# Kernel optimization log

Hardware: AMD Instinct MI355X
Metric: run time of the kernel (lower is better)

## Reference

```python
import jax, jax.numpy as jnp
import numpy as np

K = 0.1  # curvature (called k in the module)
EPS = 1e-15

def setup_inputs() -> dict:
    key = jax.random.key(0)
    k1, k2, k3 = jax.random.split(key, 3)
    B, C, D = 2048, 1000, 64
    x = jax.random.normal(k1, (B, D), dtype=jnp.float32) * 0.05  # inside ball
    a_vals = jax.random.normal(k2, (C, D), dtype=jnp.float32) * 0.05
    p_vals = jax.random.normal(k3, (C, D), dtype=jnp.float32) * 0.05
    return {"x": x, "a_vals": a_vals, "p_vals": p_vals}

def reference(x, a_vals, p_vals):
    k = jnp.asarray(K, dtype=x.dtype)
    sqrt_k = jnp.sqrt(k)
    # poincare_exp0: exponential map at the origin
    p_norm = jnp.maximum(jnp.linalg.norm(p_vals, axis=1, keepdims=True), EPS)  # [C,1]
    p_poin = jnp.tanh(sqrt_k * p_norm) * p_vals / (sqrt_k * p_norm)            # [C,D]
    # conformal scaling of a (as written in the module: 1 + k*||p||^2)
    p2 = jnp.sum(p_poin * p_poin, axis=1)                                      # [C]
    a_poin = a_vals * (1.0 + k * p2)[:, None]                                  # [C,D]
    # hyperbolic softmax logits
    lam = 2.0 / (1.0 - k * p2)                                                 # [C]
    a_norm = jnp.maximum(jnp.linalg.norm(a_poin, axis=1), EPS)                 # [C]
    scale = lam * a_norm / sqrt_k                                              # [C]
    # mobius addition of (-p) (+) x, batched -> [C,B,D]
    mp = -p_poin                                                               # [C,D]
    xy = jnp.einsum('cd,bd->cb', mp, x)                                        # [C,B]
    x2 = jnp.sum(mp * mp, axis=-1)[:, None]                                    # [C,1]
    y2 = jnp.sum(x * x, axis=-1)[None, :]                                      # [1,B]
    num = ((1.0 + 2.0 * k * xy + k * y2)[..., None] * mp[:, None, :]
           + (1.0 - k * x2)[..., None] * x[None, :, :])                        # [C,B,D]
    den = 1.0 + 2.0 * k * xy + (k * k) * x2 * y2                               # [C,B]
    mob = num / den[..., None]                                                 # [C,B,D]
    numer = 2.0 * sqrt_k * jnp.einsum('cbd,cd->cb', mob, a_poin)               # [C,B]
    denom = a_norm[:, None] * (1.0 - k * jnp.sum(mob * mob, axis=-1))          # [C,B]
    logits = scale[:, None] * jnp.arcsinh(numer / denom)                       # [C,B]
    return logits.T                                                            # [B,C]
```

## Files before the change

kernel.cpp:

```cpp
#include <hip/hip_runtime.h>
#include <hip/hip_bf16.h>
#include <math.h>

#define KCURV  0.1f
#define KK     0.010000001f
#define SQRT_K 0.31622776601683794f
#define TWO_SQRT_K 0.6324555320336759f
#define INV_SQRT_K 3.1622776601683795f
#define TD 64

typedef __bf16  bf16x8  __attribute__((ext_vector_type(8)));
typedef float   f32x4   __attribute__((ext_vector_type(4)));

__device__ __forceinline__ unsigned short f2bf(float f) {
    __hip_bfloat16 h = __float2bfloat16(f);
    return *(unsigned short*)&h;
}

__global__ __launch_bounds__(256) void prep_kernel(
    const float* __restrict__ a_vals, const float* __restrict__ p_vals,
    unsigned short* __restrict__ Pbf, unsigned short* __restrict__ Abf,
    float* __restrict__ x2g, float* __restrict__ pag,
    float* __restrict__ ang, float* __restrict__ scg,
    int C)
{
    const int tid  = threadIdx.x;
    const int item = blockIdx.x * 64 + (tid >> 2);
    const int q    = tid & 3;
    const int gc   = item < C ? item : C - 1;

    const float* pr = p_vals + (size_t)gc * TD + q * 16;
    const float* ar = a_vals + (size_t)gc * TD + q * 16;
    float pv[16], av[16];
    #pragma unroll
    for (int m = 0; m < 4; ++m) {
        *(float4*)&pv[m * 4] = *(const float4*)(pr + m * 4);
        *(float4*)&av[m * 4] = *(const float4*)(ar + m * 4);
    }
    float s_pp = 0.f, s_aa = 0.f, s_pa = 0.f;
    #pragma unroll
    for (int u = 0; u < 16; ++u) {
        s_pp = fmaf(pv[u], pv[u], s_pp);
        s_aa = fmaf(av[u], av[u], s_aa);
        s_pa = fmaf(pv[u], av[u], s_pa);
    }
    s_pp += __shfl_xor(s_pp, 1, 64); s_pp += __shfl_xor(s_pp, 2, 64);
    s_aa += __shfl_xor(s_aa, 1, 64); s_aa += __shfl_xor(s_aa, 2, 64);
    s_pa += __shfl_xor(s_pa, 1, 64); s_pa += __shfl_xor(s_pa, 2, 64);

    float pn = sqrtf(s_pp); if (pn < 1e-15f) pn = 1e-15f;
    float arg = SQRT_K * pn;
    float t = tanhf(arg);
    float factor = t / arg;
    float p2 = factor * factor * s_pp;
    float ca = 1.0f + KCURV * p2;
    float anorm = ca * sqrtf(s_aa); if (anorm < 1e-15f) anorm = 1e-15f;
    float lam = 2.0f / (1.0f - KCURV * p2);
    float scale = lam * anorm * INV_SQRT_K;
    float pa = -factor * ca * s_pa;

    if (q == 0) {
        x2g[item] = p2; pag[item] = pa; ang[item] = anorm; scg[item] = scale;
    }
    unsigned short ubp[16], uba[16];
    #pragma unroll
    for (int u = 0; u < 16; ++u) {
        ubp[u] = f2bf(-factor * pv[u]);
        uba[u] = f2bf(ca * av[u]);
    }
    unsigned short* dp = Pbf + (size_t)item * TD + q * 16;
    unsigned short* da = Abf + (size_t)item * TD + q * 16;
    *(ulonglong2*)dp       = *(const ulonglong2*)&ubp[0];
    *(ulonglong2*)(dp + 8) = *(const ulonglong2*)&ubp[8];
    *(ulonglong2*)da       = *(const ulonglong2*)&uba[0];
    *(ulonglong2*)(da + 8) = *(const ulonglong2*)&uba[8];
}

__global__ __launch_bounds__(256) void mlr_gemm_kernel(
    const float* __restrict__ x,
    const unsigned short* __restrict__ Pbf, const unsigned short* __restrict__ Abf,
    const float* __restrict__ x2g, const float* __restrict__ pag,
    const float* __restrict__ ang, const float* __restrict__ scg,
    float* __restrict__ out, int B, int C)
{
    const int tid  = threadIdx.x;
    const int w    = tid >> 6;
    const int lane = tid & 63;
    const int m16  = lane & 15;
    const int quad = lane >> 4;
    const int cb   = blockIdx.x * 64;
    const int rb   = blockIdx.y * 64;
    int arow = rb + 16 * w + m16; if (arow >= B) arow = B - 1;

    float xv[2][8];
    bf16x8 bp[4][2], ba[4][2];
    #pragma unroll
    for (int step = 0; step < 2; ++step) {
        const int ko = quad * 8 + step * 32;
        const float* xr = x + (size_t)arow * TD + ko;
        *(float4*)&xv[step][0] = *(const float4*)xr;
        *(float4*)&xv[step][4] = *(const float4*)(xr + 4);
        #pragma unroll
        for (int t = 0; t < 4; ++t) {
            const size_t crow = (size_t)(cb + 16 * t + m16) * TD + ko;
            bp[t][step] = *(const bf16x8*)(Pbf + crow);
            ba[t][step] = *(const bf16x8*)(Abf + crow);
        }
    }

    float s = 0.f;
    #pragma unroll
    for (int step = 0; step < 2; ++step)
        #pragma unroll
        for (int u = 0; u < 8; ++u) s = fmaf(xv[step][u], xv[step][u], s);
    s += __shfl_xor(s, 16, 64);
    s += __shfl_xor(s, 32, 64);
    float y2r[4];
    #pragma unroll
    for (int r = 0; r < 4; ++r) y2r[r] = __shfl(s, quad * 4 + r, 64);

    bf16x8 af[2];
    #pragma unroll
    for (int step = 0; step < 2; ++step) {
        union { unsigned short u[8]; bf16x8 v; } cv;
        #pragma unroll
        for (int u = 0; u < 8; ++u) cv.u[u] = f2bf(xv[step][u]);
        af[step] = cv.v;
    }

    f32x4 accP[4], accA[4];
    #pragma unroll
    for (int t = 0; t < 4; ++t) {
        accP[t] = (f32x4){0.f, 0.f, 0.f, 0.f};
        accA[t] = (f32x4){0.f, 0.f, 0.f, 0.f};
    }
    #pragma unroll
    for (int step = 0; step < 2; ++step) {
        #pragma unroll
        for (int t = 0; t < 4; ++t) {
            accP[t] = __builtin_amdgcn_mfma_f32_16x16x32_bf16(af[step], bp[t][step], accP[t], 0, 0, 0);
            accA[t] = __builtin_amdgcn_mfma_f32_16x16x32_bf16(af[step], ba[t][step], accA[t], 0, 0, 0);
        }
    }

    #pragma unroll
    for (int t = 0; t < 4; ++t) {
        const int cl = cb + 16 * t + m16;
        const float x2 = x2g[cl], pa = pag[cl], an = ang[cl], sc = scg[cl];
        const float beta = 1.0f - KCURV * x2;
        const float kkx2 = KK * x2;
        #pragma unroll
        for (int r = 0; r < 4; ++r) {
            const int gr = rb + 16 * w + quad * 4 + r;
            const float y2 = y2r[r];
            const float xy = accP[t][r];
            const float xa = accA[t][r];
            float t1    = fmaf(2.0f * KCURV, xy, 1.0f);
            float den   = fmaf(kkx2, y2, t1);
            float alpha = fmaf(KCURV, y2, t1);
            float g     = fmaf(alpha, pa, beta * xa);
            float M     = fmaf(alpha * alpha, x2,
                          fmaf(2.0f * alpha * beta, xy, beta * beta * y2));
            float dd    = fmaf(den, den, -KCURV * M);
            float z     = TWO_SQRT_K * g * den * __builtin_amdgcn_rcpf(an * dd);
            float lg    = sc * __logf(z + sqrtf(fmaf(z, z, 1.0f)));
            if (cl < C && gr < B) out[(size_t)gr * C + cl] = lg;
        }
    }
}

extern "C" void kernel_launch(void* const* d_in, const int* in_sizes, int n_in,
                              void* d_out, int out_size, void* d_ws, size_t ws_size,
                              hipStream_t stream) {
    const float* x      = (const float*)d_in[0];
    const float* a_vals = (const float*)d_in[1];
    const float* p_vals = (const float*)d_in[2];
    const int B = in_sizes[0] / TD;
    const int C = in_sizes[1] / TD;
    const int rowBlocks = (B + 63) / 64;
    const int clsBlocks = (C + 63) / 64;
    const int CPAD = clsBlocks * 64;

    char* ws = (char*)d_ws;
    unsigned short* Pbf = (unsigned short*)ws;
    unsigned short* Abf = (unsigned short*)(ws + (size_t)CPAD * TD * 2);
    float* x2g = (float*)(ws + (size_t)CPAD * TD * 4);
    float* pag = x2g + CPAD;
    float* ang = pag + CPAD;
    float* scg = ang + CPAD;

    prep_kernel<<<clsBlocks, 256, 0, stream>>>(
        a_vals, p_vals, Pbf, Abf, x2g, pag, ang, scg, C);

    dim3 grid(clsBlocks, rowBlocks);
    mlr_gemm_kernel<<<grid, dim3(256), 0, stream>>>(
        x, Pbf, Abf, x2g, pag, ang, scg, (float*)d_out, B, C);
}
```

Measured before the change: 70.17 us.

## Fuse class-parameter prep into GEMM kernel, removing separate prep launch

Removes the separate prep kernel and its workspace round-trip. Each GEMM block now loads the fp32 p/a rows itself, computes the norms, tanh factor and scalars, and converts to bf16 in registers. tanhf is replaced by an exp/rcp formula with a small-argument series. This drops one launch and the global writes and reads of the intermediates. In exchange every one of the 32 row-blocks recomputes the same class prep, and each wave repeats it, adding redundant fp32 loads and ALU work.

```diff
diff --git a/kernel.cpp b/kernel.cpp
--- a/kernel.cpp
+++ b/kernel.cpp
@@ -17,70 +17,10 @@
     return *(unsigned short*)&h;
 }
 
-__global__ __launch_bounds__(256) void prep_kernel(
-    const float* __restrict__ a_vals, const float* __restrict__ p_vals,
-    unsigned short* __restrict__ Pbf, unsigned short* __restrict__ Abf,
-    float* __restrict__ x2g, float* __restrict__ pag,
-    float* __restrict__ ang, float* __restrict__ scg,
-    int C)
-{
-    const int tid  = threadIdx.x;
-    const int item = blockIdx.x * 64 + (tid >> 2);
-    const int q    = tid & 3;
-    const int gc   = item < C ? item : C - 1;
-
-    const float* pr = p_vals + (size_t)gc * TD + q * 16;
-    const float* ar = a_vals + (size_t)gc * TD + q * 16;
-    float pv[16], av[16];
-    #pragma unroll
-    for (int m = 0; m < 4; ++m) {
-        *(float4*)&pv[m * 4] = *(const float4*)(pr + m * 4);
-        *(float4*)&av[m * 4] = *(const float4*)(ar + m * 4);
-    }
-    float s_pp = 0.f, s_aa = 0.f, s_pa = 0.f;
-    #pragma unroll
-    for (int u = 0; u < 16; ++u) {
-        s_pp = fmaf(pv[u], pv[u], s_pp);
-        s_aa = fmaf(av[u], av[u], s_aa);
-        s_pa = fmaf(pv[u], av[u], s_pa);
-    }
-    s_pp += __shfl_xor(s_pp, 1, 64); s_pp += __shfl_xor(s_pp, 2, 64);
-    s_aa += __shfl_xor(s_aa, 1, 64); s_aa += __shfl_xor(s_aa, 2, 64);
-    s_pa += __shfl_xor(s_pa, 1, 64); s_pa += __shfl_xor(s_pa, 2, 64);
-
-    float pn = sqrtf(s_pp); if (pn < 1e-15f) pn = 1e-15f;
-    float arg = SQRT_K * pn;
-    float t = tanhf(arg);
-    float factor = t / arg;
-    float p2 = factor * factor * s_pp;
-    float ca = 1.0f + KCURV * p2;
-    float anorm = ca * sqrtf(s_aa); if (anorm < 1e-15f) anorm = 1e-15f;
-    float lam = 2.0f / (1.0f - KCURV * p2);
-    float scale = lam * anorm * INV_SQRT_K;
-    float pa = -factor * ca * s_pa;
-
-    if (q == 0) {
-        x2g[item] = p2; pag[item] = pa; ang[item] = anorm; scg[item] = scale;
-    }
-    unsigned short ubp[16], uba[16];
-    #pragma unroll
-    for (int u = 0; u < 16; ++u) {
-        ubp[u] = f2bf(-factor * pv[u]);
-        uba[u] = f2bf(ca * av[u]);
-    }
-    unsigned short* dp = Pbf + (size_t)item * TD + q * 16;
-    unsigned short* da = Abf + (size_t)item * TD + q * 16;
-    *(ulonglong2*)dp       = *(const ulonglong2*)&ubp[0];
-    *(ulonglong2*)(dp + 8) = *(const ulonglong2*)&ubp[8];
-    *(ulonglong2*)da       = *(const ulonglong2*)&uba[0];
-    *(ulonglong2*)(da + 8) = *(const ulonglong2*)&uba[8];
-}
-
-__global__ __launch_bounds__(256) void mlr_gemm_kernel(
+__global__ __launch_bounds__(256) void fused_mlr_kernel(
     const float* __restrict__ x,
-    const unsigned short* __restrict__ Pbf, const unsigned short* __restrict__ Abf,
-    const float* __restrict__ x2g, const float* __restrict__ pag,
-    const float* __restrict__ ang, const float* __restrict__ scg,
+    const float* __restrict__ a_vals,
+    const float* __restrict__ p_vals,
     float* __restrict__ out, int B, int C)
 {
     const int tid  = threadIdx.x;
@@ -93,19 +33,67 @@
     int arow = rb + 16 * w + m16; if (arow >= B) arow = B - 1;
 
     float xv[2][8];
-    bf16x8 bp[4][2], ba[4][2];
     #pragma unroll
     for (int step = 0; step < 2; ++step) {
         const int ko = quad * 8 + step * 32;
         const float* xr = x + (size_t)arow * TD + ko;
         *(float4*)&xv[step][0] = *(const float4*)xr;
         *(float4*)&xv[step][4] = *(const float4*)(xr + 4);
+    }
+
+    bf16x8 bp[4][2], ba[4][2];
+    float x2s[4], pas[4], ans[4], scs[4];
+    #pragma unroll
+    for (int t = 0; t < 4; ++t) {
+        int c = cb + 16 * t + m16; if (c >= C) c = C - 1;
+        const float* pr = p_vals + (size_t)c * TD + quad * 8;
+        const float* ar = a_vals + (size_t)c * TD + quad * 8;
+        float pv[16], av[16];
+        *(float4*)&pv[0]  = *(const float4*)pr;
+        *(float4*)&pv[4]  = *(const float4*)(pr + 4);
+        *(float4*)&pv[8]  = *(const float4*)(pr + 32);
+        *(float4*)&pv[12] = *(const float4*)(pr + 36);
+        *(float4*)&av[0]  = *(const float4*)ar;
+        *(float4*)&av[4]  = *(const float4*)(ar + 4);
+        *(float4*)&av[8]  = *(const float4*)(ar + 32);
+        *(float4*)&av[12] = *(const float4*)(ar + 36);
+
+        float s_pp = 0.f, s_aa = 0.f, s_pa = 0.f;
         #pragma unroll
-        for (int t = 0; t < 4; ++t) {
-            const size_t crow = (size_t)(cb + 16 * t + m16) * TD + ko;
-            bp[t][step] = *(const bf16x8*)(Pbf + crow);
-            ba[t][step] = *(const bf16x8*)(Abf + crow);
+        for (int u = 0; u < 16; ++u) {
+            s_pp = fmaf(pv[u], pv[u], s_pp);
+            s_aa = fmaf(av[u], av[u], s_aa);
+            s_pa = fmaf(pv[u], av[u], s_pa);
         }
+        s_pp += __shfl_xor(s_pp, 16, 64); s_pp += __shfl_xor(s_pp, 32, 64);
+        s_aa += __shfl_xor(s_aa, 16, 64); s_aa += __shfl_xor(s_aa, 32, 64);
+        s_pa += __shfl_xor(s_pa, 16, 64); s_pa += __shfl_xor(s_pa, 32, 64);
+
+        float pn = sqrtf(s_pp); if (pn < 1e-15f) pn = 1e-15f;
+        float arg = SQRT_K * pn;
+        float e2 = __expf(2.0f * arg);
+        float th = (e2 - 1.0f) * __builtin_amdgcn_rcpf(e2 + 1.0f);
+        float factor = (arg > 1e-4f) ? th * __builtin_amdgcn_rcpf(arg)
+                                     : 1.0f - 0.333333333f * arg * arg;
+        float p2 = factor * factor * s_pp;
+        float ca = 1.0f + KCURV * p2;
+        float anorm = ca * sqrtf(s_aa); if (anorm < 1e-15f) anorm = 1e-15f;
+        float lam = 2.0f * __builtin_amdgcn_rcpf(1.0f - KCURV * p2);
+        x2s[t] = p2;
+        pas[t] = -factor * ca * s_pa;
+        ans[t] = anorm;
+        scs[t] = lam * anorm * INV_SQRT_K;
+
+        union { unsigned short u[8]; bf16x8 v; } c0, c1, d0, d1;
+        #pragma unroll
+        for (int u = 0; u < 8; ++u) {
+            c0.u[u] = f2bf(-factor * pv[u]);
+            c1.u[u] = f2bf(-factor * pv[8 + u]);
+            d0.u[u] = f2bf(ca * av[u]);
+            d1.u[u] = f2bf(ca * av[8 + u]);
+        }
+        bp[t][0] = c0.v; bp[t][1] = c1.v;
+        ba[t][0] = d0.v; ba[t][1] = d1.v;
     }
 
     float s = 0.f;
@@ -146,7 +134,7 @@
     #pragma unroll
     for (int t = 0; t < 4; ++t) {
         const int cl = cb + 16 * t + m16;
-        const float x2 = x2g[cl], pa = pag[cl], an = ang[cl], sc = scg[cl];
+        const float x2 = x2s[t], pa = pas[t], an = ans[t], sc = scs[t];
         const float beta = 1.0f - KCURV * x2;
         const float kkx2 = KK * x2;
         #pragma unroll
@@ -179,20 +167,8 @@
     const int C = in_sizes[1] / TD;
     const int rowBlocks = (B + 63) / 64;
     const int clsBlocks = (C + 63) / 64;
-    const int CPAD = clsBlocks * 64;
-
-    char* ws = (char*)d_ws;
-    unsigned short* Pbf = (unsigned short*)ws;
-    unsigned short* Abf = (unsigned short*)(ws + (size_t)CPAD * TD * 2);
-    float* x2g = (float*)(ws + (size_t)CPAD * TD * 4);
-    float* pag = x2g + CPAD;
-    float* ang = pag + CPAD;
-    float* scg = ang + CPAD;
-
-    prep_kernel<<<clsBlocks, 256, 0, stream>>>(
-        a_vals, p_vals, Pbf, Abf, x2g, pag, ang, scg, C);
 
     dim3 grid(clsBlocks, rowBlocks);
-    mlr_gemm_kernel<<<grid, dim3(256), 0, stream>>>(
-        x, Pbf, Abf, x2g, pag, ang, scg, (float*)d_out, B, C);
+    fused_mlr_kernel<<<grid, dim3(256), 0, stream>>>(
+        x, a_vals, p_vals, (float*)d_out, B, C);
 }
```

Result: slower. 75.06 us (+7.0%).
